# Performance work log

Measured on AMD Instinct MI355X. Metric: run time of the kernel, lower is better.

The kernel has to match this reference:

```python
import jax, jax.numpy as jnp
import numpy as np

B, N, C = 256, 25, 256          # batch, joints, in_features
H = 256                          # hidden_features (MLP hidden = H // 2 = 128)


def _build_chain_paths(n):
    """Flatten shortest paths of a chain skeleton (parent[i]=i-1) into
    (heads, ends, pair_ids): edge k of path i->j contributes
    src[:, ends[e]] - src[:, heads[e]] accumulated into pair i*n+j."""
    heads, ends, pair = [], [], []
    for i in range(n):
        for j in range(n):
            step = 1 if j >= i else -1
            cur = i
            while cur != j:
                heads.append(cur)
                ends.append(cur + step)
                pair.append(i * n + j)
                cur += step
    return (np.asarray(heads, np.int32), np.asarray(ends, np.int32),
            np.asarray(pair, np.int32))


def setup_inputs() -> dict:
    key = jax.random.key(0)
    k_src, k_w1, k_w2 = jax.random.split(key, 3)
    heads, ends, pair_ids = _build_chain_paths(N)  # E = 5200 for N=25
    src = jax.random.normal(k_src, (B, N, C), dtype=jnp.float32)
    # torch Linear weights: [out, in], no bias for both edgefeat linears
    W1 = jax.random.normal(k_w1, (H // 2, C), dtype=jnp.float32) / np.sqrt(C)
    W2 = jax.random.normal(k_w2, (1, H // 2), dtype=jnp.float32) / np.sqrt(H // 2)
    alpha = jnp.full((1,), 0.25, dtype=jnp.float32)  # PReLU init
    return {"src": src, "heads": jnp.asarray(heads), "ends": jnp.asarray(ends),
            "pair_ids": jnp.asarray(pair_ids), "W1": W1, "alpha": alpha, "W2": W2}


def reference(src, heads, ends, pair_ids, W1, alpha, W2):
    b, n, c = src.shape
    # gather-subtract along every path edge: [B, E, C]
    diff = src[:, ends, :] - src[:, heads, :]
    # accumulate per (i, j) pair: segment_sum over leading axis -> [N*N, B, C]
    acc = jax.ops.segment_sum(jnp.transpose(diff, (1, 0, 2)), pair_ids,
                              num_segments=n * n)
    edge_feat = jnp.transpose(acc.reshape(n, n, b, c), (2, 0, 1, 3))  # [B,N,N,C]
    h = jnp.einsum('bijc,hc->bijh', edge_feat, W1)   # [B,N,N,H//2]
    h = jnp.where(h >= 0, h, alpha * h)              # PReLU (single shared alpha)
    return jnp.einsum('bijh,oh->bijo', h, W2)        # [B,N,N,1]
```

## Files before the change

kernel.cpp:

```cpp
#include <hip/hip_runtime.h>

#define NJ    25
#define CIN   256
#define HH    128
#define AS    264

typedef __attribute__((ext_vector_type(8))) short short8;
typedef __attribute__((ext_vector_type(4))) float f32x4;

__device__ __forceinline__ unsigned short f2bf(float f) {
    union { float f; unsigned u; } v; v.f = f;
    unsigned r = v.u + 0x7FFF + ((v.u >> 16) & 1);
    return (unsigned short)(r >> 16);
}
__device__ __forceinline__ float bf2f(short s) {
    union { unsigned u; float f; } v;
    v.u = ((unsigned)(unsigned short)s) << 16;
    return v.f;
}

__global__ __launch_bounds__(512) void fused_edge_mlp_mfma(
    const float* __restrict__ src,
    const float* __restrict__ W1,
    const float* __restrict__ Aarr,
    const float* __restrict__ W2,
    float* __restrict__ out)
{
    __shared__ short a_s[32 * AS];
    __shared__ short u8s[16 * 26 * 8];

    const int b = blockIdx.x;
    const int t = threadIdx.x;

    {
        unsigned* au = (unsigned*)a_s;
        for (int i = (25 * AS) / 2 + t; i < (32 * AS) / 2; i += 512) au[i] = 0u;
        const float4* s4 = reinterpret_cast<const float4*>(src) + (long)b * (NJ * CIN / 4);
        for (int idx = t; idx < NJ * CIN / 4; idx += 512) {
            int n  = idx >> 6;
            int k4 = idx & 63;
            float4 v = s4[idx];
            unsigned lo = (unsigned)f2bf(v.x) | ((unsigned)f2bf(v.y) << 16);
            unsigned hi = (unsigned)f2bf(v.z) | ((unsigned)f2bf(v.w) << 16);
            uint2* dst = (uint2*)&a_s[n * AS + k4 * 4];
            *dst = make_uint2(lo, hi);
        }
    }
    __syncthreads();

    {
        const int w    = t >> 6;
        const int lane = t & 63;
        const int ln15 = lane & 15;
        const int quad = lane >> 4;
        const int hcol = w * 16 + ln15;

        short8 bfrag[8];
        const float* w1row = W1 + hcol * CIN;
        #pragma unroll
        for (int kt = 0; kt < 8; ++kt) {
            const float* p = w1row + kt * 32 + quad * 8;
            float4 x = *reinterpret_cast<const float4*>(p);
            float4 y = *reinterpret_cast<const float4*>(p + 4);
            short8 bf;
            bf[0] = (short)f2bf(x.x); bf[1] = (short)f2bf(x.y);
            bf[2] = (short)f2bf(x.z); bf[3] = (short)f2bf(x.w);
            bf[4] = (short)f2bf(y.x); bf[5] = (short)f2bf(y.y);
            bf[6] = (short)f2bf(y.z); bf[7] = (short)f2bf(y.w);
            bfrag[kt] = bf;
        }

        f32x4 acc0 = {0.f, 0.f, 0.f, 0.f};
        f32x4 acc1 = {0.f, 0.f, 0.f, 0.f};
        #pragma unroll
        for (int kt = 0; kt < 8; ++kt) {
            const int ko = kt * 32 + quad * 8;
            short8 a0 = *reinterpret_cast<const short8*>(&a_s[(ln15)      * AS + ko]);
            short8 a1 = *reinterpret_cast<const short8*>(&a_s[(16 + ln15) * AS + ko]);
            acc0 = __builtin_amdgcn_mfma_f32_16x16x32_bf16(a0, bfrag[kt], acc0, 0, 0, 0);
            acc1 = __builtin_amdgcn_mfma_f32_16x16x32_bf16(a1, bfrag[kt], acc1, 0, 0, 0);
        }

        const int h8  = hcol >> 3;
        const int hlo = hcol & 7;
        #pragma unroll
        for (int r = 0; r < 4; ++r) {
            int m0 = quad * 4 + r;
            if (m0 < NJ) u8s[(h8 * 26 + m0) * 8 + hlo] = (short)f2bf(acc0[r]);
            int m1 = 16 + quad * 4 + r;
            if (m1 < NJ) u8s[(h8 * 26 + m1) * 8 + hlo] = (short)f2bf(acc1[r]);
        }
    }
    __syncthreads();

    const float alpha = Aarr[0];
    float* outb = out + (long)b * (NJ * NJ);

    for (int p = t; p < NJ * NJ; p += 512) {
        int i = p / NJ;
        int j = p - i * NJ;
        float accS = 0.f, accP = 0.f;
        #pragma unroll 4
        for (int h8 = 0; h8 < 16; ++h8) {
            short8 uj = *reinterpret_cast<const short8*>(&u8s[(h8 * 26 + j) * 8]);
            short8 ui = *reinterpret_cast<const short8*>(&u8s[(h8 * 26 + i) * 8]);
            const float* w2p = W2 + h8 * 8;
            #pragma unroll
            for (int q = 0; q < 8; ++q) {
                float d = bf2f(uj[q]) - bf2f(ui[q]);
                float w = w2p[q];
                accS = fmaf(w, d, accS);
                accP = fmaf(w, fmaxf(d, 0.f), accP);
            }
        }
        outb[p] = accP + alpha * (accS - accP);
    }
}

extern "C" void kernel_launch(void* const* d_in, const int* in_sizes, int n_in,
                              void* d_out, int out_size, void* d_ws, size_t ws_size,
                              hipStream_t stream) {
    const float* src   = (const float*)d_in[0];
    const float* W1    = (const float*)d_in[4];
    const float* alpha = (const float*)d_in[5];
    const float* W2    = (const float*)d_in[6];
    float* out = (float*)d_out;

    const int B = in_sizes[0] / (NJ * CIN);
    fused_edge_mlp_mfma<<<B, 512, 0, stream>>>(src, W1, alpha, W2, out);
}
```

Baseline: 75.73 us.

## Exploit pair antisymmetry and split each batch across two blocks

The epilogue now computes only the upper-triangular (i<j) pairs. It uses max(ui,uj) and the per-row sums to produce both out[i,j] and out[j,i] from one pass, and writes zeros on the diagonal. The grid doubles, with two blocks per batch element each taking half of the 300 pairs. This cuts the per-pair PReLU/W2 work roughly in half and adds parallelism, but each of the two blocks redundantly reloads src and recomputes the full first GEMM.

```diff
diff --git a/kernel.cpp b/kernel.cpp
--- a/kernel.cpp
+++ b/kernel.cpp
@@ -4,6 +4,8 @@
 #define CIN   256
 #define HH    128
 #define AS    264
+#define NPAIR 300
+#define HALFP 150
 
 typedef __attribute__((ext_vector_type(8))) short short8;
 typedef __attribute__((ext_vector_type(4))) float f32x4;
@@ -19,7 +21,7 @@
     return v.f;
 }
 
-__global__ __launch_bounds__(512) void fused_edge_mlp_mfma(
+__global__ __launch_bounds__(512) void fused_edge_mlp_v3(
     const float* __restrict__ src,
     const float* __restrict__ W1,
     const float* __restrict__ Aarr,
@@ -29,8 +31,9 @@
     __shared__ short a_s[32 * AS];
     __shared__ short u8s[16 * 26 * 8];
 
-    const int b = blockIdx.x;
-    const int t = threadIdx.x;
+    const int b    = blockIdx.x >> 1;
+    const int hb   = blockIdx.x & 1;
+    const int t    = threadIdx.x;
 
     {
         unsigned* au = (unsigned*)a_s;
@@ -42,8 +45,7 @@
             float4 v = s4[idx];
             unsigned lo = (unsigned)f2bf(v.x) | ((unsigned)f2bf(v.y) << 16);
             unsigned hi = (unsigned)f2bf(v.z) | ((unsigned)f2bf(v.w) << 16);
-            uint2* dst = (uint2*)&a_s[n * AS + k4 * 4];
-            *dst = make_uint2(lo, hi);
+            *(uint2*)&a_s[n * AS + k4 * 4] = make_uint2(lo, hi);
         }
     }
     __syncthreads();
@@ -96,24 +98,39 @@
     const float alpha = Aarr[0];
     float* outb = out + (long)b * (NJ * NJ);
 
-    for (int p = t; p < NJ * NJ; p += 512) {
-        int i = p / NJ;
-        int j = p - i * NJ;
-        float accS = 0.f, accP = 0.f;
+    if (t < HALFP) {
+        const int p = hb * HALFP + t;
+        int i = (int)((49.0f - sqrtf(2401.0f - 8.0f * (float)p)) * 0.5f);
+        {
+            int Si = (49 * i - i * i) >> 1;
+            if (p < Si) { --i; }
+            else { int Sn = (49 * (i + 1) - (i + 1) * (i + 1)) >> 1; if (p >= Sn) ++i; }
+        }
+        const int S  = (49 * i - i * i) >> 1;
+        const int j  = p - S + i + 1;
+
+        float M = 0.f, sj = 0.f, si = 0.f;
         #pragma unroll 4
         for (int h8 = 0; h8 < 16; ++h8) {
-            short8 uj = *reinterpret_cast<const short8*>(&u8s[(h8 * 26 + j) * 8]);
-            short8 ui = *reinterpret_cast<const short8*>(&u8s[(h8 * 26 + i) * 8]);
+            short8 uj8 = *reinterpret_cast<const short8*>(&u8s[(h8 * 26 + j) * 8]);
+            short8 ui8 = *reinterpret_cast<const short8*>(&u8s[(h8 * 26 + i) * 8]);
             const float* w2p = W2 + h8 * 8;
             #pragma unroll
             for (int q = 0; q < 8; ++q) {
-                float d = bf2f(uj[q]) - bf2f(ui[q]);
-                float w = w2p[q];
-                accS = fmaf(w, d, accS);
-                accP = fmaf(w, fmaxf(d, 0.f), accP);
+                float fj = bf2f(uj8[q]);
+                float fi = bf2f(ui8[q]);
+                float w  = w2p[q];
+                M  = fmaf(w, fmaxf(fi, fj), M);
+                sj = fmaf(w, fj, sj);
+                si = fmaf(w, fi, si);
             }
         }
-        outb[p] = accP + alpha * (accS - accP);
+        const float Mw = (1.f - alpha) * M;
+        outb[i * NJ + j] = Mw + alpha * sj - si;
+        outb[j * NJ + i] = Mw + alpha * si - sj;
+    } else if (hb == 0 && t < HALFP + NJ) {
+        const int i = t - HALFP;
+        outb[i * NJ + i] = 0.f;
     }
 }
 
@@ -127,5 +144,5 @@
     float* out = (float*)d_out;
 
     const int B = in_sizes[0] / (NJ * CIN);
-    fused_edge_mlp_mfma<<<B, 512, 0, stream>>>(src, W1, alpha, W2, out);
+    fused_edge_mlp_v3<<<B * 2, 512, 0, stream>>>(src, W1, alpha, W2, out);
 }
```

After: 78.98 us. 1.04x slower.

## Prepack bf16 MFMA fragments in a prep kernel and exploit pair antisymmetry

Applied to the files above, without the earlier changes.

Adds a separate kernel that converts src and W1 into bf16 fragments laid out in MFMA lane order in workspace, so the main kernel loads fragments directly from global memory instead of staging through LDS. The epilogue keeps fp32 per-joint projections and uses the identity relu(a-b) = max(a,b)-b to compute each unordered (i,j) pair once, writing both out[i,j] and out[j,i] and zeroing the diagonal. This removes LDS staging and halves the epilogue arithmetic, at the cost of an extra launch and a global round trip for the converted src.

```diff
diff --git a/kernel.cpp b/kernel.cpp
--- a/kernel.cpp
+++ b/kernel.cpp
@@ -1,9 +1,8 @@
 #include <hip/hip_runtime.h>
 
-#define NJ    25
-#define CIN   256
-#define HH    128
-#define AS    264
+#define NJ   25
+#define CIN  256
+#define HH   128
 
 typedef __attribute__((ext_vector_type(8))) short short8;
 typedef __attribute__((ext_vector_type(4))) float f32x4;
@@ -13,107 +12,121 @@
     unsigned r = v.u + 0x7FFF + ((v.u >> 16) & 1);
     return (unsigned short)(r >> 16);
 }
-__device__ __forceinline__ float bf2f(short s) {
-    union { unsigned u; float f; } v;
-    v.u = ((unsigned)(unsigned short)s) << 16;
-    return v.f;
+__device__ __forceinline__ unsigned pack2(float a, float b) {
+    return (unsigned)f2bf(a) | ((unsigned)f2bf(b) << 16);
 }
 
-__global__ __launch_bounds__(512) void fused_edge_mlp_mfma(
-    const float* __restrict__ src,
-    const float* __restrict__ W1,
+__global__ __launch_bounds__(256) void prep_frags(
+    const float* __restrict__ src, const float* __restrict__ W1,
+    unsigned short* __restrict__ srcfrag, unsigned short* __restrict__ w1frag,
+    int nsrc)
+{
+    const int gid = blockIdx.x * 256 + threadIdx.x;
+    const float* base;
+    unsigned short* dst;
+    if (gid < nsrc) {
+        const int lane = gid & 63, kt = (gid >> 6) & 7, mt = (gid >> 9) & 1, b = gid >> 10;
+        const int row = mt * 16 + (lane & 15);
+        const int k0  = kt * 32 + (lane >> 4) * 8;
+        dst = srcfrag + (size_t)gid * 8;
+        if (row >= NJ) { *(uint4*)dst = make_uint4(0u, 0u, 0u, 0u); return; }
+        base = src + ((size_t)b * NJ + row) * CIN + k0;
+    } else {
+        const int id = gid - nsrc;
+        if (id >= 4096) return;
+        const int lane = id & 63, kt = (id >> 6) & 7, nt = id >> 9;
+        const int row = nt * 16 + (lane & 15);
+        const int k0  = kt * 32 + (lane >> 4) * 8;
+        dst = w1frag + (size_t)id * 8;
+        base = W1 + (size_t)row * CIN + k0;
+    }
+    float4 x = *(const float4*)base;
+    float4 y = *(const float4*)(base + 4);
+    uint4 o;
+    o.x = pack2(x.x, x.y); o.y = pack2(x.z, x.w);
+    o.z = pack2(y.x, y.y); o.w = pack2(y.z, y.w);
+    *(uint4*)dst = o;
+}
+
+__global__ __launch_bounds__(512) void fused_edge_mlp_v4(
+    const unsigned short* __restrict__ srcfrag,
+    const unsigned short* __restrict__ w1frag,
     const float* __restrict__ Aarr,
     const float* __restrict__ W2,
     float* __restrict__ out)
 {
-    __shared__ short a_s[32 * AS];
-    __shared__ short u8s[16 * 26 * 8];
+    __shared__ float u_s[NJ * 132];
 
-    const int b = blockIdx.x;
-    const int t = threadIdx.x;
+    const int b    = blockIdx.x;
+    const int t    = threadIdx.x;
+    const int w    = t >> 6;
+    const int lane = t & 63;
+    const int ln15 = lane & 15;
+    const int quad = lane >> 4;
 
     {
-        unsigned* au = (unsigned*)a_s;
-        for (int i = (25 * AS) / 2 + t; i < (32 * AS) / 2; i += 512) au[i] = 0u;
-        const float4* s4 = reinterpret_cast<const float4*>(src) + (long)b * (NJ * CIN / 4);
-        for (int idx = t; idx < NJ * CIN / 4; idx += 512) {
-            int n  = idx >> 6;
-            int k4 = idx & 63;
-            float4 v = s4[idx];
-            unsigned lo = (unsigned)f2bf(v.x) | ((unsigned)f2bf(v.y) << 16);
-            unsigned hi = (unsigned)f2bf(v.z) | ((unsigned)f2bf(v.w) << 16);
-            uint2* dst = (uint2*)&a_s[n * AS + k4 * 4];
-            *dst = make_uint2(lo, hi);
-        }
-    }
-    __syncthreads();
-
-    {
-        const int w    = t >> 6;
-        const int lane = t & 63;
-        const int ln15 = lane & 15;
-        const int quad = lane >> 4;
-        const int hcol = w * 16 + ln15;
+        const short8* w1p = (const short8*)w1frag + (w * 8) * 64 + lane;
+        const short8* ap  = (const short8*)srcfrag + ((size_t)b * 16) * 64 + lane;
 
         short8 bfrag[8];
-        const float* w1row = W1 + hcol * CIN;
         #pragma unroll
-        for (int kt = 0; kt < 8; ++kt) {
-            const float* p = w1row + kt * 32 + quad * 8;
-            float4 x = *reinterpret_cast<const float4*>(p);
-            float4 y = *reinterpret_cast<const float4*>(p + 4);
-            short8 bf;
-            bf[0] = (short)f2bf(x.x); bf[1] = (short)f2bf(x.y);
-            bf[2] = (short)f2bf(x.z); bf[3] = (short)f2bf(x.w);
-            bf[4] = (short)f2bf(y.x); bf[5] = (short)f2bf(y.y);
-            bf[6] = (short)f2bf(y.z); bf[7] = (short)f2bf(y.w);
-            bfrag[kt] = bf;
-        }
+        for (int kt = 0; kt < 8; ++kt) bfrag[kt] = w1p[kt * 64];
 
         f32x4 acc0 = {0.f, 0.f, 0.f, 0.f};
         f32x4 acc1 = {0.f, 0.f, 0.f, 0.f};
         #pragma unroll
         for (int kt = 0; kt < 8; ++kt) {
-            const int ko = kt * 32 + quad * 8;
-            short8 a0 = *reinterpret_cast<const short8*>(&a_s[(ln15)      * AS + ko]);
-            short8 a1 = *reinterpret_cast<const short8*>(&a_s[(16 + ln15) * AS + ko]);
+            short8 a0 = ap[kt * 64];
+            short8 a1 = ap[(8 + kt) * 64];
             acc0 = __builtin_amdgcn_mfma_f32_16x16x32_bf16(a0, bfrag[kt], acc0, 0, 0, 0);
             acc1 = __builtin_amdgcn_mfma_f32_16x16x32_bf16(a1, bfrag[kt], acc1, 0, 0, 0);
         }
 
-        const int h8  = hcol >> 3;
-        const int hlo = hcol & 7;
+        const int hcol = w * 16 + ln15;
         #pragma unroll
         for (int r = 0; r < 4; ++r) {
             int m0 = quad * 4 + r;
-            if (m0 < NJ) u8s[(h8 * 26 + m0) * 8 + hlo] = (short)f2bf(acc0[r]);
+            if (m0 < NJ) u_s[m0 * 132 + hcol] = acc0[r];
             int m1 = 16 + quad * 4 + r;
-            if (m1 < NJ) u8s[(h8 * 26 + m1) * 8 + hlo] = (short)f2bf(acc1[r]);
+            if (m1 < NJ) u_s[m1 * 132 + hcol] = acc1[r];
         }
     }
     __syncthreads();
 
     const float alpha = Aarr[0];
-    float* outb = out + (long)b * (NJ * NJ);
+    float* outb = out + (size_t)b * (NJ * NJ);
 
-    for (int p = t; p < NJ * NJ; p += 512) {
-        int i = p / NJ;
-        int j = p - i * NJ;
-        float accS = 0.f, accP = 0.f;
-        #pragma unroll 4
-        for (int h8 = 0; h8 < 16; ++h8) {
-            short8 uj = *reinterpret_cast<const short8*>(&u8s[(h8 * 26 + j) * 8]);
-            short8 ui = *reinterpret_cast<const short8*>(&u8s[(h8 * 26 + i) * 8]);
-            const float* w2p = W2 + h8 * 8;
-            #pragma unroll
-            for (int q = 0; q < 8; ++q) {
-                float d = bf2f(uj[q]) - bf2f(ui[q]);
-                float w = w2p[q];
-                accS = fmaf(w, d, accS);
-                accP = fmaf(w, fmaxf(d, 0.f), accP);
-            }
+    if (t < 300) {
+        int i = (int)((49.0f - sqrtf(2401.0f - 8.0f * (float)t)) * 0.5f);
+        {
+            int Si = (49 * i - i * i) >> 1;
+            if (t < Si) { --i; }
+            else { int Sn = (49 * (i + 1) - (i + 1) * (i + 1)) >> 1; if (t >= Sn) ++i; }
         }
-        outb[p] = accP + alpha * (accS - accP);
+        const int S = (49 * i - i * i) >> 1;
+        const int j = t - S + i + 1;
+
+        const float* uj = u_s + j * 132;
+        const float* ui = u_s + i * 132;
+        const float4* w2v = (const float4*)W2;
+
+        float M = 0.f, sj = 0.f, si = 0.f;
+        #pragma unroll 8
+        for (int h4 = 0; h4 < 32; ++h4) {
+            float4 a = *(const float4*)(uj + h4 * 4);
+            float4 c = *(const float4*)(ui + h4 * 4);
+            float4 ww = w2v[h4];
+            M  = fmaf(ww.x, fmaxf(a.x, c.x), M); sj = fmaf(ww.x, a.x, sj); si = fmaf(ww.x, c.x, si);
+            M  = fmaf(ww.y, fmaxf(a.y, c.y), M); sj = fmaf(ww.y, a.y, sj); si = fmaf(ww.y, c.y, si);
+            M  = fmaf(ww.z, fmaxf(a.z, c.z), M); sj = fmaf(ww.z, a.z, sj); si = fmaf(ww.z, c.z, si);
+            M  = fmaf(ww.w, fmaxf(a.w, c.w), M); sj = fmaf(ww.w, a.w, sj); si = fmaf(ww.w, c.w, si);
+        }
+        const float Mw = (1.f - alpha) * M;
+        outb[i * NJ + j] = Mw + alpha * sj - si;
+        outb[j * NJ + i] = Mw + alpha * si - sj;
+    } else if (t < 325) {
+        const int i = t - 300;
+        outb[i * (NJ + 1)] = 0.f;
     }
 }
 
@@ -126,6 +139,12 @@
     const float* W2    = (const float*)d_in[6];
     float* out = (float*)d_out;
 
-    const int B = in_sizes[0] / (NJ * CIN);
-    fused_edge_mlp_mfma<<<B, 512, 0, stream>>>(src, W1, alpha, W2, out);
+    const int B    = in_sizes[0] / (NJ * CIN);
+    const int nsrc = B * 16 * 64;
+    unsigned short* srcfrag = (unsigned short*)d_ws;
+    unsigned short* w1frag  = srcfrag + (size_t)nsrc * 8;
+
+    const int totalA = nsrc + 4096;
+    prep_frags<<<(totalA + 255) / 256, 256, 0, stream>>>(src, W1, srcfrag, w1frag, nsrc);
+    fused_edge_mlp_v4<<<B, 512, 0, stream>>>(srcfrag, w1frag, alpha, W2, out);
 }
```

New measurement: 74.62 us. No clear change (-1.5%).
